# Optimization experiments

Hardware: AMD Instinct MI355X
Metric: run time of the kernel (lower is better)

## Reference

```python
import jax, jax.numpy as jnp
import numpy as np

EPS = 1e-8

def l2norm(x, axis=-1):
    norm = jnp.sqrt(jnp.sum(x * x, axis=axis, keepdims=True)) + EPS
    return x / norm

def setup_inputs() -> dict:
    key = jax.random.key(0)
    ks = jax.random.split(key, 4)
    B, Lq, Ls, d, sim_dim = 128, 128, 256, 1024, 256
    query = jax.random.normal(ks[0], (B, Lq, d), dtype=jnp.float32)
    context = jax.random.normal(ks[1], (B, Ls, d), dtype=jnp.float32)
    matrix = jax.random.uniform(ks[2], (B, Lq, d), dtype=jnp.float32)
    W = jax.random.normal(ks[3], (sim_dim, d), dtype=jnp.float32) * (1.0 / np.sqrt(d))
    b = jnp.zeros((sim_dim,), dtype=jnp.float32)
    smooth = 9
    return {"query": query, "context": context, "matrix": matrix, "W": W, "b": b, "smooth": smooth}

def reference(query, context, matrix, W, b, smooth):
    # cross_attention
    q = query * matrix                                   # (B, Lq, d)
    attn = jnp.einsum('bsd,bqd->bsq', context, q)        # (B, Ls, Lq)
    attn = jnp.where(attn >= 0, attn, 0.1 * attn)        # LeakyReLU(0.1)
    attn = l2norm(attn, axis=-1)                         # normalize over Lq
    attn = jnp.swapaxes(attn, 1, 2)                      # (B, Lq, Ls)
    attn = jax.nn.softmax(attn * smooth, axis=2)         # softmax over source
    wcontext = jnp.einsum('bqs,bsd->bqd', attn, context) # (B, Lq, d)
    wcontext = l2norm(wcontext, axis=-1)
    # alignment vector
    sim_rep = (query - wcontext) ** 2                    # (B, Lq, d)
    sim_rep = jnp.einsum('bqd,kd->bqk', sim_rep, W) + b  # Linear d -> sim_dim
    sim_rep = l2norm(sim_rep, axis=-1)
    return sim_rep
```

## Files before the change

kernel.cpp:

```cpp
#include <hip/hip_runtime.h>
#include <hip/hip_bf16.h>

constexpr int B  = 128;
constexpr int LQ = 128;
constexpr int LS = 256;
constexpr int D  = 1024;
constexpr int SD = 256;
constexpr float EPS = 1e-8f;

typedef __attribute__((ext_vector_type(8))) __bf16 bf16x8;
typedef __attribute__((ext_vector_type(4))) float f32x4;

__device__ inline ushort f2bf(float f) {
    union { float f; uint u; } v{f};
    uint r = v.u + 0x7fffu + ((v.u >> 16) & 1u);
    return (ushort)(r >> 16);
}
__device__ inline float bf2f(ushort u) {
    union { uint u; float f; } v{(uint)u << 16};
    return v.f;
}
__device__ inline uint4 pack8(float4 a, float4 b) {
    union { ushort us[8]; uint4 u4; } r;
    r.us[0]=f2bf(a.x); r.us[1]=f2bf(a.y); r.us[2]=f2bf(a.z); r.us[3]=f2bf(a.w);
    r.us[4]=f2bf(b.x); r.us[5]=f2bf(b.y); r.us[6]=f2bf(b.z); r.us[7]=f2bf(b.w);
    return r.u4;
}
__device__ inline int swz(int row, int kbyte) {
    return row * 128 + (kbyte ^ ((row & 7) << 4));
}
__device__ inline bf16x8 lds_frag(const ushort* base, int row, int kk, int lane) {
    int kbyte = kk * 64 + (lane >> 4) * 16;
    return *(const bf16x8*)((const char*)base + swz(row, kbyte));
}
__device__ inline int swz512(int row, int kbyte) {
    return row * 512 + (kbyte ^ ((row & 7) << 4));
}
__device__ inline f32x4 mfma16(bf16x8 a, bf16x8 b, f32x4 c) {
    return __builtin_amdgcn_mfma_f32_16x16x32_bf16(a, b, c, 0, 0, 0);
}

__global__ __launch_bounds__(256) void wconv_kernel(
    const float* __restrict__ W, ushort* __restrict__ Wb)
{
    size_t i = ((size_t)blockIdx.x * 256 + threadIdx.x) * 8;
    float4 a = *(const float4*)(W + i);
    float4 b = *(const float4*)(W + i + 4);
    *(uint4*)(Wb + i) = pack8(a, b);
}

__global__ __launch_bounds__(512, 2) void gemmA_kernel(
    const float* __restrict__ query, const float* __restrict__ mat,
    const float* __restrict__ ctx, const int* __restrict__ smooth_p,
    ushort* __restrict__ E)
{
    const int bid = blockIdx.x;
    const int xcd = bid & 7, idx = bid >> 3;
    const int b  = xcd * 16 + (idx >> 1);
    const int n0 = (idx & 1) * 128;
    __shared__ ushort SH[4][128 * 64];
    __shared__ float colssP[2][128];
    __shared__ float invsm[128];
    ushort* Et = &SH[0][0];

    const int t = threadIdx.x;
    const int wv = t >> 6, l = t & 63;
    const int wq = wv >> 2, wsv = wv & 3;

    const float* Qb = query + (size_t)b * LQ * D;
    const float* Mb = mat   + (size_t)b * LQ * D;
    const float* Cb = ctx   + ((size_t)b * LS + n0) * D;
    const int r0 = t >> 3, k8 = (t & 7) * 8;

    f32x4 acc[4][2] = {};
    float4 q0,q1,q2,q3, m0,m1,m2,m3, c0,c1,c2,c3;

    auto loadT = [&](int k0) {
        const float* qp = Qb + (size_t)r0 * D + k0 + k8;
        const float* mp = Mb + (size_t)r0 * D + k0 + k8;
        q0 = *(const float4*)qp; q1 = *(const float4*)(qp + 4);
        m0 = *(const float4*)mp; m1 = *(const float4*)(mp + 4);
        qp += (size_t)64 * D;  mp += (size_t)64 * D;
        q2 = *(const float4*)qp; q3 = *(const float4*)(qp + 4);
        m2 = *(const float4*)mp; m3 = *(const float4*)(mp + 4);
        const float* cp = Cb + (size_t)r0 * D + k0 + k8;
        c0 = *(const float4*)cp; c1 = *(const float4*)(cp + 4);
        cp += (size_t)64 * D;
        c2 = *(const float4*)cp; c3 = *(const float4*)(cp + 4);
    };
    auto storeT = [&](int buf) {
        float4 p1{q0.x*m0.x, q0.y*m0.y, q0.z*m0.z, q0.w*m0.w};
        float4 p2{q1.x*m1.x, q1.y*m1.y, q1.z*m1.z, q1.w*m1.w};
        *(uint4*)((char*)&SH[buf][0] + swz(r0, k8 * 2)) = pack8(p1, p2);
        float4 p3{q2.x*m2.x, q2.y*m2.y, q2.z*m2.z, q2.w*m2.w};
        float4 p4{q3.x*m3.x, q3.y*m3.y, q3.z*m3.z, q3.w*m3.w};
        *(uint4*)((char*)&SH[buf][0] + swz(r0 + 64, k8 * 2)) = pack8(p3, p4);
        *(uint4*)((char*)&SH[2 + buf][0] + swz(r0, k8 * 2))      = pack8(c0, c1);
        *(uint4*)((char*)&SH[2 + buf][0] + swz(r0 + 64, k8 * 2)) = pack8(c2, c3);
    };
    auto mfmaT = [&](int buf) {
#pragma unroll
        for (int kk = 0; kk < 2; ++kk) {
            bf16x8 bfr0 = lds_frag(&SH[2 + buf][0], wsv * 32 + (l & 15), kk, l);
            bf16x8 bfr1 = lds_frag(&SH[2 + buf][0], wsv * 32 + 16 + (l & 15), kk, l);
#pragma unroll
            for (int i = 0; i < 4; ++i) {
                bf16x8 af = lds_frag(&SH[buf][0], wq * 64 + i * 16 + (l & 15), kk, l);
                acc[i][0] = mfma16(af, bfr0, acc[i][0]);
                acc[i][1] = mfma16(af, bfr1, acc[i][1]);
            }
        }
    };

    loadT(0);
    storeT(0);
    __syncthreads();
    int cur = 0;
#pragma unroll 1
    for (int ks = 0; ks < 15; ++ks) {
        loadT((ks + 1) * 64);
        mfmaT(cur);
        storeT(cur ^ 1);
        __syncthreads();
        cur ^= 1;
    }
    mfmaT(cur);

#pragma unroll
    for (int n = 0; n < 2; ++n) {
        float csum = 0.f;
#pragma unroll
        for (int i = 0; i < 4; ++i)
#pragma unroll
            for (int r = 0; r < 4; ++r) {
                float v = acc[i][n][r];
                v = v >= 0.f ? v : 0.1f * v;
                acc[i][n][r] = v;
                csum += v * v;
            }
        csum += __shfl_xor(csum, 16);
        csum += __shfl_xor(csum, 32);
        if (l < 16) colssP[wq][wsv * 32 + n * 16 + l] = csum;
    }
    __syncthreads();
    const float sm = (float)(*smooth_p);
    if (t < 128) invsm[t] = sm / (sqrtf(colssP[0][t] + colssP[1][t]) + EPS);
    __syncthreads();
#pragma unroll
    for (int n = 0; n < 2; ++n) {
        const float invc = invsm[wsv * 32 + n * 16 + (l & 15)];
#pragma unroll
        for (int i = 0; i < 4; ++i)
#pragma unroll
            for (int r = 0; r < 4; ++r) {
                int row = wq * 64 + i * 16 + (l >> 4) * 4 + r;
                Et[row * 136 + wsv * 32 + n * 16 + (l & 15)] =
                    f2bf(__expf(acc[i][n][r] * invc));
            }
    }
    __syncthreads();
    ushort* Eg = E + (size_t)b * LQ * LS + n0;
#pragma unroll
    for (int j = 0; j < 4; ++j) {
        int c = t + j * 512;
        int row = c >> 4, s8 = (c & 15) * 8;
        *(uint4*)(Eg + (size_t)row * LS + s8) = *(const uint4*)(Et + row * 136 + s8);
    }
}

__global__ __launch_bounds__(512, 2) void pv_kernel(
    const ushort* __restrict__ E, const float* __restrict__ ctx,
    ushort* __restrict__ wctx, float* __restrict__ rowssP)
{
    const int bid = blockIdx.x;
    const int xcd = bid & 7, idx = bid >> 3;
    const int b  = xcd * 16 + (idx >> 1);
    const int dh = idx & 1;
    const int dglob0 = dh * 512;

    __shared__ ushort Es[128 * 256];
    __shared__ ushort Bs[64 * 264];
    __shared__ float rsumL[128];
    __shared__ float rinv[128];
    __shared__ float rowssL[128][4];

    const int t = threadIdx.x;
    const int wv = t >> 6, l = t & 63;
    const int wq = wv >> 2, wd = wv & 3;

    const ushort* Eb = E + (size_t)b * LQ * LS;
    const int cc = t & 31, rr = t >> 5;
    float part[8];
#pragma unroll
    for (int p = 0; p < 8; ++p) {
        int row = rr + p * 16;
        uint4 v = *(const uint4*)(Eb + (size_t)row * LS + cc * 8);
        *(uint4*)((char*)Es + swz512(row, cc * 16)) = v;
        const ushort* us = (const ushort*)&v;
        float s = 0.f;
#pragma unroll
        for (int j = 0; j < 8; ++j) s += bf2f(us[j]);
        part[p] = s;
    }
    rowssL[t >> 2][t & 3] = 0.f;
#pragma unroll
    for (int p = 0; p < 8; ++p) {
        float s = part[p];
        s += __shfl_xor(s, 1);  s += __shfl_xor(s, 2);
        s += __shfl_xor(s, 4);  s += __shfl_xor(s, 8);
        s += __shfl_xor(s, 16);
        if ((l & 31) == 0) rsumL[rr + p * 16] = s;
    }

    const float* Cb = ctx + (size_t)b * LS * D + dglob0;
    const int sr = t >> 4, c4 = (t & 15) * 4;
    float4 cr[8];
#pragma unroll
    for (int p = 0; p < 8; ++p)
        cr[p] = *(const float4*)(Cb + (size_t)(p * 32 + sr) * D + c4);

    __syncthreads();
    if (t < 128) rinv[t] = 1.0f / rsumL[t];

#pragma unroll
    for (int p = 0; p < 8; ++p) {
        int s = p * 32 + sr;
        Bs[(c4 + 0) * 264 + s] = f2bf(cr[p].x);
        Bs[(c4 + 1) * 264 + s] = f2bf(cr[p].y);
        Bs[(c4 + 2) * 264 + s] = f2bf(cr[p].z);
        Bs[(c4 + 3) * 264 + s] = f2bf(cr[p].w);
    }
    __syncthreads();

    ushort* Ob = wctx + (size_t)b * LQ * D + dglob0;

#pragma unroll 1
    for (int dt = 0; dt < 8; ++dt) {
        if (dt < 7) {
#pragma unroll
            for (int p = 0; p < 8; ++p)
                cr[p] = *(const float4*)(Cb + (size_t)(p * 32 + sr) * D + (dt + 1) * 64 + c4);
        }
        f32x4 acc[4] = {};
#pragma unroll
        for (int kk = 0; kk < 8; ++kk) {
            const ushort* bp = Bs + (wd * 16 + (l & 15)) * 264 + kk * 32 + (l >> 4) * 8;
            bf16x8 bfr = *(const bf16x8*)bp;
#pragma unroll
            for (int i = 0; i < 4; ++i) {
                bf16x8 af = *(const bf16x8*)((const char*)Es +
                    swz512(wq * 64 + i * 16 + (l & 15), kk * 64 + (l >> 4) * 16));
                acc[i] = mfma16(af, bfr, acc[i]);
            }
        }
#pragma unroll
        for (int i = 0; i < 4; ++i)
#pragma unroll
            for (int r = 0; r < 4; ++r) {
                int row = wq * 64 + i * 16 + (l >> 4) * 4 + r;
                float wval = acc[i][r] * rinv[row];
                float p2 = wval * wval;
                p2 += __shfl_xor(p2, 1); p2 += __shfl_xor(p2, 2);
                p2 += __shfl_xor(p2, 4); p2 += __shfl_xor(p2, 8);
                if ((l & 15) == 0) rowssL[row][wd] += p2;
                Ob[(size_t)row * D + dt * 64 + wd * 16 + (l & 15)] = f2bf(wval);
            }
        __syncthreads();
        if (dt < 7) {
#pragma unroll
            for (int p = 0; p < 8; ++p) {
                int s = p * 32 + sr;
                Bs[(c4 + 0) * 264 + s] = f2bf(cr[p].x);
                Bs[(c4 + 1) * 264 + s] = f2bf(cr[p].y);
                Bs[(c4 + 2) * 264 + s] = f2bf(cr[p].z);
                Bs[(c4 + 3) * 264 + s] = f2bf(cr[p].w);
            }
            __syncthreads();
        }
    }
    if (t < 128)
        rowssP[(size_t)b * 256 + dh * 128 + t] =
            rowssL[t][0] + rowssL[t][1] + rowssL[t][2] + rowssL[t][3];
}

__global__ __launch_bounds__(512, 2) void gemm3_kernel(
    const ushort* __restrict__ wctx, const float* __restrict__ query,
    const float* __restrict__ rowssP, const ushort* __restrict__ Wb,
    const float* __restrict__ bias, float* __restrict__ out)
{
    const int m0 = blockIdx.x * 64;
    const int b  = blockIdx.y;
    __shared__ ushort As[64 * 64];
    __shared__ ushort Bs[256 * 64];
    __shared__ float red[64][4];
    __shared__ float invr[64];
    const int t = threadIdx.x;
    const int w = t >> 6, l = t & 63;
    const int wm = (w >> 2) * 32, wn = (w & 3) * 64;

    const int arow = t >> 3, ako = (t & 7) * 8;
    const float r0v = rowssP[(size_t)b * 256 + m0 + arow];
    const float r1v = rowssP[(size_t)b * 256 + 128 + m0 + arow];
    const float ivq = 1.0f / (sqrtf(r0v + r1v) + EPS);
    const float* Qp  = query + ((size_t)b * LQ + m0 + arow) * D + ako;
    const ushort* Wp = wctx  + ((size_t)b * LQ + m0 + arow) * D + ako;

    f32x4 acc[2][4] = {};

    for (int k0 = 0; k0 < D; k0 += 64) {
        if (k0) __syncthreads();
        {
            uint4 wu = *(const uint4*)(Wp + k0);
            float4 q1 = *(const float4*)(Qp + k0);
            float4 q2 = *(const float4*)(Qp + k0 + 4);
            float d0 = q1.x - bf2f((ushort)(wu.x & 0xffff)) * ivq;
            float d1 = q1.y - bf2f((ushort)(wu.x >> 16))    * ivq;
            float d2 = q1.z - bf2f((ushort)(wu.y & 0xffff)) * ivq;
            float d3 = q1.w - bf2f((ushort)(wu.y >> 16))    * ivq;
            float d4 = q2.x - bf2f((ushort)(wu.z & 0xffff)) * ivq;
            float d5 = q2.y - bf2f((ushort)(wu.z >> 16))    * ivq;
            float d6 = q2.z - bf2f((ushort)(wu.w & 0xffff)) * ivq;
            float d7 = q2.w - bf2f((ushort)(wu.w >> 16))    * ivq;
            float4 s1{d0*d0, d1*d1, d2*d2, d3*d3};
            float4 s2{d4*d4, d5*d5, d6*d6, d7*d7};
            *(uint4*)((char*)As + swz(arow, ako * 2)) = pack8(s1, s2);
        }
#pragma unroll
        for (int j = 0; j < 4; ++j) {
            int c = t + j * 512;
            int row = c >> 3, ko = (c & 7) * 8;
            *(uint4*)((char*)Bs + swz(row, ko * 2)) =
                *(const uint4*)(Wb + (size_t)row * D + k0 + ko);
        }
        __syncthreads();
#pragma unroll
        for (int kk = 0; kk < 2; ++kk) {
            bf16x8 af[2], bfr[4];
#pragma unroll
            for (int i = 0; i < 2; ++i) af[i] = lds_frag(As, wm + i * 16 + (l & 15), kk, l);
#pragma unroll
            for (int n = 0; n < 4; ++n) bfr[n] = lds_frag(Bs, wn + n * 16 + (l & 15), kk, l);
#pragma unroll
            for (int i = 0; i < 2; ++i)
#pragma unroll
                for (int n = 0; n < 4; ++n) acc[i][n] = mfma16(af[i], bfr[n], acc[i][n]);
        }
    }
#pragma unroll
    for (int n = 0; n < 4; ++n) {
        float bv = bias[wn + n * 16 + (l & 15)];
#pragma unroll
        for (int i = 0; i < 2; ++i)
#pragma unroll
            for (int r = 0; r < 4; ++r) acc[i][n][r] += bv;
    }
#pragma unroll
    for (int i = 0; i < 2; ++i)
#pragma unroll
        for (int r = 0; r < 4; ++r) {
            float p = 0.f;
#pragma unroll
            for (int n = 0; n < 4; ++n) p += acc[i][n][r] * acc[i][n][r];
#pragma unroll
            for (int off = 1; off < 16; off <<= 1) p += __shfl_xor(p, off);
            int rowl = wm + i * 16 + (l >> 4) * 4 + r;
            if ((l & 15) == 0) red[rowl][w & 3] = p;
        }
    __syncthreads();
    if (t < 64) {
        float s = red[t][0] + red[t][1] + red[t][2] + red[t][3];
        invr[t] = 1.0f / (sqrtf(s) + EPS);
    }
    __syncthreads();
    float* Ob = out + ((size_t)b * LQ + m0) * SD;
#pragma unroll
    for (int i = 0; i < 2; ++i)
#pragma unroll
        for (int r = 0; r < 4; ++r) {
            int rowl = wm + i * 16 + (l >> 4) * 4 + r;
            float iv = invr[rowl];
#pragma unroll
            for (int n = 0; n < 4; ++n) {
                int col = wn + n * 16 + (l & 15);
                Ob[(size_t)rowl * SD + col] = acc[i][n][r] * iv;
            }
        }
}

extern "C" void kernel_launch(void* const* d_in, const int* in_sizes, int n_in,
                              void* d_out, int out_size, void* d_ws, size_t ws_size,
                              hipStream_t stream)
{
    const float* query  = (const float*)d_in[0];
    const float* ctx    = (const float*)d_in[1];
    const float* mat    = (const float*)d_in[2];
    const float* W      = (const float*)d_in[3];
    const float* bias   = (const float*)d_in[4];
    const int*   smooth = (const int*)d_in[5];
    float* out = (float*)d_out;

    char* ws = (char*)d_ws;
    ushort* wctx   = (ushort*)ws;
    ushort* E      = (ushort*)(ws + (size_t)32 * 1024 * 1024);
    ushort* Wb     = (ushort*)(ws + (size_t)40 * 1024 * 1024);
    float*  rowssP = (float*)(ws + (size_t)(40 * 1024 + 512) * 1024);

    wconv_kernel<<<dim3(SD * D / (256 * 8)), 256, 0, stream>>>(W, Wb);
    gemmA_kernel<<<dim3(256), 512, 0, stream>>>(query, mat, ctx, smooth, E);
    pv_kernel<<<dim3(256), 512, 0, stream>>>(E, ctx, wctx, rowssP);
    gemm3_kernel<<<dim3(2, B), 512, 0, stream>>>(wctx, query, rowssP, Wb, bias, out);
}
```

Before: 149.8 us.

## Split gemmA over K into 512 blocks, add combine kernel, reuse bf16 context

```diff
diff --git a/kernel.cpp b/kernel.cpp
--- a/kernel.cpp
+++ b/kernel.cpp
@@ -51,26 +51,28 @@
 
 __global__ __launch_bounds__(512, 2) void gemmA_kernel(
     const float* __restrict__ query, const float* __restrict__ mat,
-    const float* __restrict__ ctx, const int* __restrict__ smooth_p,
-    ushort* __restrict__ E)
+    const float* __restrict__ ctx, float* __restrict__ Spart,
+    ushort* __restrict__ ctxB)
 {
     const int bid = blockIdx.x;
     const int xcd = bid & 7, idx = bid >> 3;
-    const int b  = xcd * 16 + (idx >> 1);
-    const int n0 = (idx & 1) * 128;
+    const int b   = xcd * 16 + (idx >> 2);
+    const int sub = idx & 3;
+    const int sh  = sub >> 1;
+    const int kh  = sub & 1;
+    const int n0    = sh * 128;
+    const int kbase = kh * 512;
     __shared__ ushort SH[4][128 * 64];
-    __shared__ float colssP[2][128];
-    __shared__ float invsm[128];
-    ushort* Et = &SH[0][0];
 
     const int t = threadIdx.x;
+
+    const float* Qb = query + (size_t)b * LQ * D + kbase;
+    const float* Mb = mat   + (size_t)b * LQ * D + kbase;
+    const float* Cb = ctx   + ((size_t)b * LS + n0) * D + kbase;
+    ushort*     CBb = ctxB  + ((size_t)b * LS + n0) * D + kbase;
+    const int r0 = t >> 3, k8 = (t & 7) * 8;
     const int wv = t >> 6, l = t & 63;
     const int wq = wv >> 2, wsv = wv & 3;
-
-    const float* Qb = query + (size_t)b * LQ * D;
-    const float* Mb = mat   + (size_t)b * LQ * D;
-    const float* Cb = ctx   + ((size_t)b * LS + n0) * D;
-    const int r0 = t >> 3, k8 = (t & 7) * 8;
 
     f32x4 acc[4][2] = {};
     float4 q0,q1,q2,q3, m0,m1,m2,m3, c0,c1,c2,c3;
@@ -88,15 +90,19 @@
         cp += (size_t)64 * D;
         c2 = *(const float4*)cp; c3 = *(const float4*)(cp + 4);
     };
-    auto storeT = [&](int buf) {
+    auto storeT = [&](int buf, int kc) {
         float4 p1{q0.x*m0.x, q0.y*m0.y, q0.z*m0.z, q0.w*m0.w};
         float4 p2{q1.x*m1.x, q1.y*m1.y, q1.z*m1.z, q1.w*m1.w};
         *(uint4*)((char*)&SH[buf][0] + swz(r0, k8 * 2)) = pack8(p1, p2);
         float4 p3{q2.x*m2.x, q2.y*m2.y, q2.z*m2.z, q2.w*m2.w};
         float4 p4{q3.x*m3.x, q3.y*m3.y, q3.z*m3.z, q3.w*m3.w};
         *(uint4*)((char*)&SH[buf][0] + swz(r0 + 64, k8 * 2)) = pack8(p3, p4);
-        *(uint4*)((char*)&SH[2 + buf][0] + swz(r0, k8 * 2))      = pack8(c0, c1);
-        *(uint4*)((char*)&SH[2 + buf][0] + swz(r0 + 64, k8 * 2)) = pack8(c2, c3);
+        uint4 pc0 = pack8(c0, c1);
+        uint4 pc1 = pack8(c2, c3);
+        *(uint4*)((char*)&SH[2 + buf][0] + swz(r0, k8 * 2))      = pc0;
+        *(uint4*)((char*)&SH[2 + buf][0] + swz(r0 + 64, k8 * 2)) = pc1;
+        *(uint4*)(CBb + (size_t)r0 * D + kc + k8)        = pc0;
+        *(uint4*)(CBb + (size_t)(r0 + 64) * D + kc + k8) = pc1;
     };
     auto mfmaT = [&](int buf) {
 #pragma unroll
@@ -113,18 +119,53 @@
     };
 
     loadT(0);
-    storeT(0);
+    storeT(0, 0);
     __syncthreads();
     int cur = 0;
 #pragma unroll 1
-    for (int ks = 0; ks < 15; ++ks) {
+    for (int ks = 0; ks < 7; ++ks) {
         loadT((ks + 1) * 64);
         mfmaT(cur);
-        storeT(cur ^ 1);
+        storeT(cur ^ 1, (ks + 1) * 64);
         __syncthreads();
         cur ^= 1;
     }
     mfmaT(cur);
+
+    float* Sp = Spart + (((size_t)(b * 2 + sh) * 2 + kh) * 512 + t) * 32;
+#pragma unroll
+    for (int i = 0; i < 4; ++i)
+#pragma unroll
+        for (int n = 0; n < 2; ++n)
+            *(f32x4*)(Sp + (i * 2 + n) * 4) = acc[i][n];
+}
+
+__global__ __launch_bounds__(512, 2) void combine_kernel(
+    const float* __restrict__ Spart, const int* __restrict__ smooth_p,
+    ushort* __restrict__ E)
+{
+    const int bid = blockIdx.x;
+    const int xcd = bid & 7, idx = bid >> 3;
+    const int b  = xcd * 16 + (idx >> 1);
+    const int sh = idx & 1;
+    __shared__ float colssP[2][128];
+    __shared__ float invsm[128];
+    __shared__ ushort Et[128 * 136];
+
+    const int t = threadIdx.x;
+    const int wv = t >> 6, l = t & 63;
+    const int wq = wv >> 2, wsv = wv & 3;
+
+    const float* S0 = Spart + (((size_t)(b * 2 + sh) * 2 + 0) * 512 + t) * 32;
+    const float* S1 = Spart + (((size_t)(b * 2 + sh) * 2 + 1) * 512 + t) * 32;
+
+    f32x4 acc[4][2];
+#pragma unroll
+    for (int i = 0; i < 4; ++i)
+#pragma unroll
+        for (int n = 0; n < 2; ++n)
+            acc[i][n] = *(const f32x4*)(S0 + (i * 2 + n) * 4) +
+                        *(const f32x4*)(S1 + (i * 2 + n) * 4);
 
 #pragma unroll
     for (int n = 0; n < 2; ++n) {
@@ -159,7 +200,7 @@
             }
     }
     __syncthreads();
-    ushort* Eg = E + (size_t)b * LQ * LS + n0;
+    ushort* Eg = E + (size_t)b * LQ * LS + sh * 128;
 #pragma unroll
     for (int j = 0; j < 4; ++j) {
         int c = t + j * 512;
@@ -169,7 +210,7 @@
 }
 
 __global__ __launch_bounds__(512, 2) void pv_kernel(
-    const ushort* __restrict__ E, const float* __restrict__ ctx,
+    const ushort* __restrict__ E, const ushort* __restrict__ ctxB,
     ushort* __restrict__ wctx, float* __restrict__ rowssP)
 {
     const int bid = blockIdx.x;
@@ -212,12 +253,12 @@
         if ((l & 31) == 0) rsumL[rr + p * 16] = s;
     }
 
-    const float* Cb = ctx + (size_t)b * LS * D + dglob0;
+    const ushort* Cb = ctxB + (size_t)b * LS * D + dglob0;
     const int sr = t >> 4, c4 = (t & 15) * 4;
-    float4 cr[8];
+    uint2 cr[8];
 #pragma unroll
     for (int p = 0; p < 8; ++p)
-        cr[p] = *(const float4*)(Cb + (size_t)(p * 32 + sr) * D + c4);
+        cr[p] = *(const uint2*)(Cb + (size_t)(p * 32 + sr) * D + c4);
 
     __syncthreads();
     if (t < 128) rinv[t] = 1.0f / rsumL[t];
@@ -225,10 +266,11 @@
 #pragma unroll
     for (int p = 0; p < 8; ++p) {
         int s = p * 32 + sr;
-        Bs[(c4 + 0) * 264 + s] = f2bf(cr[p].x);
-        Bs[(c4 + 1) * 264 + s] = f2bf(cr[p].y);
-        Bs[(c4 + 2) * 264 + s] = f2bf(cr[p].z);
-        Bs[(c4 + 3) * 264 + s] = f2bf(cr[p].w);
+        const ushort* us = (const ushort*)&cr[p];
+        Bs[(c4 + 0) * 264 + s] = us[0];
+        Bs[(c4 + 1) * 264 + s] = us[1];
+        Bs[(c4 + 2) * 264 + s] = us[2];
+        Bs[(c4 + 3) * 264 + s] = us[3];
     }
     __syncthreads();
 
@@ -239,7 +281,7 @@
         if (dt < 7) {
 #pragma unroll
             for (int p = 0; p < 8; ++p)
-                cr[p] = *(const float4*)(Cb + (size_t)(p * 32 + sr) * D + (dt + 1) * 64 + c4);
+                cr[p] = *(const uint2*)(Cb + (size_t)(p * 32 + sr) * D + (dt + 1) * 64 + c4);
         }
         f32x4 acc[4] = {};
 #pragma unroll
@@ -270,10 +312,11 @@
 #pragma unroll
             for (int p = 0; p < 8; ++p) {
                 int s = p * 32 + sr;
-                Bs[(c4 + 0) * 264 + s] = f2bf(cr[p].x);
-                Bs[(c4 + 1) * 264 + s] = f2bf(cr[p].y);
-                Bs[(c4 + 2) * 264 + s] = f2bf(cr[p].z);
-                Bs[(c4 + 3) * 264 + s] = f2bf(cr[p].w);
+                const ushort* us = (const ushort*)&cr[p];
+                Bs[(c4 + 0) * 264 + s] = us[0];
+                Bs[(c4 + 1) * 264 + s] = us[1];
+                Bs[(c4 + 2) * 264 + s] = us[2];
+                Bs[(c4 + 3) * 264 + s] = us[3];
             }
             __syncthreads();
         }
@@ -400,13 +443,16 @@
     float* out = (float*)d_out;
 
     char* ws = (char*)d_ws;
-    ushort* wctx   = (ushort*)ws;
-    ushort* E      = (ushort*)(ws + (size_t)32 * 1024 * 1024);
-    ushort* Wb     = (ushort*)(ws + (size_t)40 * 1024 * 1024);
-    float*  rowssP = (float*)(ws + (size_t)(40 * 1024 + 512) * 1024);
+    ushort* ctxB   = (ushort*)ws;
+    float*  Spart  = (float*)(ws + (size_t)64 * 1024 * 1024);
+    ushort* wctx   = (ushort*)Spart;
+    ushort* E      = (ushort*)(ws + (size_t)96 * 1024 * 1024);
+    ushort* Wb     = (ushort*)(ws + (size_t)104 * 1024 * 1024);
+    float*  rowssP = (float*)(ws + (size_t)(104 * 1024 + 512) * 1024);
 
     wconv_kernel<<<dim3(SD * D / (256 * 8)), 256, 0, stream>>>(W, Wb);
-    gemmA_kernel<<<dim3(256), 512, 0, stream>>>(query, mat, ctx, smooth, E);
-    pv_kernel<<<dim3(256), 512, 0, stream>>>(E, ctx, wctx, rowssP);
+    gemmA_kernel<<<dim3(512), 512, 0, stream>>>(query, mat, ctx, Spart, ctxB);
+    combine_kernel<<<dim3(256), 512, 0, stream>>>(Spart, smooth, E);
+    pv_kernel<<<dim3(256), 512, 0, stream>>>(E, ctxB, wctx, rowssP);
     gemm3_kernel<<<dim3(2, B), 512, 0, stream>>>(wctx, query, rowssP, Wb, bias, out);
 }
```

After: 178.8 us. 1.19x slower.

## Stage fp32 tiles to LDS via async global_load_lds and convert at fragment load

Applied to the files above, without the earlier changes.

```diff
diff --git a/kernel.cpp b/kernel.cpp
--- a/kernel.cpp
+++ b/kernel.cpp
@@ -26,6 +26,12 @@
     r.us[4]=f2bf(b.x); r.us[5]=f2bf(b.y); r.us[6]=f2bf(b.z); r.us[7]=f2bf(b.w);
     return r.u4;
 }
+__device__ inline bf16x8 pack8v(float4 a, float4 b) {
+    union { ushort us[8]; bf16x8 v; } r;
+    r.us[0]=f2bf(a.x); r.us[1]=f2bf(a.y); r.us[2]=f2bf(a.z); r.us[3]=f2bf(a.w);
+    r.us[4]=f2bf(b.x); r.us[5]=f2bf(b.y); r.us[6]=f2bf(b.z); r.us[7]=f2bf(b.w);
+    return r.v;
+}
 __device__ inline int swz(int row, int kbyte) {
     return row * 128 + (kbyte ^ ((row & 7) << 4));
 }
@@ -38,6 +44,11 @@
 }
 __device__ inline f32x4 mfma16(bf16x8 a, bf16x8 b, f32x4 c) {
     return __builtin_amdgcn_mfma_f32_16x16x32_bf16(a, b, c, 0, 0, 0);
+}
+__device__ inline void gll16(const void* g, void* l) {
+    __builtin_amdgcn_global_load_lds(
+        (const __attribute__((address_space(1))) void*)g,
+        (__attribute__((address_space(3))) void*)l, 16, 0, 0);
 }
 
 __global__ __launch_bounds__(256) void wconv_kernel(
@@ -57,11 +68,13 @@
     const int bid = blockIdx.x;
     const int xcd = bid & 7, idx = bid >> 3;
     const int b  = xcd * 16 + (idx >> 1);
-    const int n0 = (idx & 1) * 128;
-    __shared__ ushort SH[4][128 * 64];
-    __shared__ float colssP[2][128];
-    __shared__ float invsm[128];
-    ushort* Et = &SH[0][0];
+    const int sh = idx & 1;
+    const int n0 = sh * 128;
+
+    __shared__ __align__(16) char SMEM[96 * 1024 + 1536];
+    float*  colssP = (float*)(SMEM + 98304);
+    float*  invsm  = (float*)(SMEM + 99328);
+    ushort* Et     = (ushort*)SMEM;
 
     const int t = threadIdx.x;
     const int wv = t >> 6, l = t & 63;
@@ -70,61 +83,63 @@
     const float* Qb = query + (size_t)b * LQ * D;
     const float* Mb = mat   + (size_t)b * LQ * D;
     const float* Cb = ctx   + ((size_t)b * LS + n0) * D;
-    const int r0 = t >> 3, k8 = (t & 7) * 8;
+
+    const int r0 = t >> 3,        cr0 = t & 7;
+    const int r1 = (t >> 3) + 64, cr1 = t & 7;
+    const int sc0 = (cr0 ^ (r0 & 7)) * 4;
+    const int sc1 = (cr1 ^ (r1 & 7)) * 4;
+
+    auto stage = [&](int buf, int k0) {
+        char* base = SMEM + buf * 49152;
+        gll16(Qb + (size_t)r0 * D + k0 + sc0, base + t * 16);
+        gll16(Qb + (size_t)r1 * D + k0 + sc1, base + (t + 512) * 16);
+        gll16(Mb + (size_t)r0 * D + k0 + sc0, base + 16384 + t * 16);
+        gll16(Mb + (size_t)r1 * D + k0 + sc1, base + 16384 + (t + 512) * 16);
+        gll16(Cb + (size_t)r0 * D + k0 + sc0, base + 32768 + t * 16);
+        gll16(Cb + (size_t)r1 * D + k0 + sc1, base + 32768 + (t + 512) * 16);
+    };
 
     f32x4 acc[4][2] = {};
-    float4 q0,q1,q2,q3, m0,m1,m2,m3, c0,c1,c2,c3;
-
-    auto loadT = [&](int k0) {
-        const float* qp = Qb + (size_t)r0 * D + k0 + k8;
-        const float* mp = Mb + (size_t)r0 * D + k0 + k8;
-        q0 = *(const float4*)qp; q1 = *(const float4*)(qp + 4);
-        m0 = *(const float4*)mp; m1 = *(const float4*)(mp + 4);
-        qp += (size_t)64 * D;  mp += (size_t)64 * D;
-        q2 = *(const float4*)qp; q3 = *(const float4*)(qp + 4);
-        m2 = *(const float4*)mp; m3 = *(const float4*)(mp + 4);
-        const float* cp = Cb + (size_t)r0 * D + k0 + k8;
-        c0 = *(const float4*)cp; c1 = *(const float4*)(cp + 4);
-        cp += (size_t)64 * D;
-        c2 = *(const float4*)cp; c3 = *(const float4*)(cp + 4);
+    const int kc = (l >> 4) * 2;
+
+    auto compute = [&](int buf) {
+        const char* SQ = SMEM + buf * 49152;
+        const char* SM = SQ + 16384;
+        const char* SC = SQ + 32768;
+        bf16x8 bfr[2];
+#pragma unroll
+        for (int n = 0; n < 2; ++n) {
+            int S = wsv * 32 + n * 16 + (l & 15);
+            float4 cA = *(const float4*)(SC + S * 128 + ((kc ^ (S & 7)) * 16));
+            float4 cB = *(const float4*)(SC + S * 128 + (((kc + 1) ^ (S & 7)) * 16));
+            bfr[n] = pack8v(cA, cB);
+        }
+#pragma unroll
+        for (int i = 0; i < 4; ++i) {
+            int R = wq * 64 + i * 16 + (l & 15);
+            float4 qA = *(const float4*)(SQ + R * 128 + ((kc ^ (R & 7)) * 16));
+            float4 qB = *(const float4*)(SQ + R * 128 + (((kc + 1) ^ (R & 7)) * 16));
+            float4 mA = *(const float4*)(SM + R * 128 + ((kc ^ (R & 7)) * 16));
+            float4 mB = *(const float4*)(SM + R * 128 + (((kc + 1) ^ (R & 7)) * 16));
+            float4 pA{qA.x*mA.x, qA.y*mA.y, qA.z*mA.z, qA.w*mA.w};
+            float4 pB{qB.x*mB.x, qB.y*mB.y, qB.z*mB.z, qB.w*mB.w};
+            bf16x8 af = pack8v(pA, pB);
+            acc[i][0] = mfma16(af, bfr[0], acc[i][0]);
+            acc[i][1] = mfma16(af, bfr[1], acc[i][1]);
+        }
     };
-    auto storeT = [&](int buf) {
-        float4 p1{q0.x*m0.x, q0.y*m0.y, q0.z*m0.z, q0.w*m0.w};
-        float4 p2{q1.x*m1.x, q1.y*m1.y, q1.z*m1.z, q1.w*m1.w};
-        *(uint4*)((char*)&SH[buf][0] + swz(r0, k8 * 2)) = pack8(p1, p2);
-        float4 p3{q2.x*m2.x, q2.y*m2.y, q2.z*m2.z, q2.w*m2.w};
-        float4 p4{q3.x*m3.x, q3.y*m3.y, q3.z*m3.z, q3.w*m3.w};
-        *(uint4*)((char*)&SH[buf][0] + swz(r0 + 64, k8 * 2)) = pack8(p3, p4);
-        *(uint4*)((char*)&SH[2 + buf][0] + swz(r0, k8 * 2))      = pack8(c0, c1);
-        *(uint4*)((char*)&SH[2 + buf][0] + swz(r0 + 64, k8 * 2)) = pack8(c2, c3);
-    };
-    auto mfmaT = [&](int buf) {
-#pragma unroll
-        for (int kk = 0; kk < 2; ++kk) {
-            bf16x8 bfr0 = lds_frag(&SH[2 + buf][0], wsv * 32 + (l & 15), kk, l);
-            bf16x8 bfr1 = lds_frag(&SH[2 + buf][0], wsv * 32 + 16 + (l & 15), kk, l);
-#pragma unroll
-            for (int i = 0; i < 4; ++i) {
-                bf16x8 af = lds_frag(&SH[buf][0], wq * 64 + i * 16 + (l & 15), kk, l);
-                acc[i][0] = mfma16(af, bfr0, acc[i][0]);
-                acc[i][1] = mfma16(af, bfr1, acc[i][1]);
-            }
-        }
-    };
-
-    loadT(0);
-    storeT(0);
+
+    stage(0, 0);
     __syncthreads();
     int cur = 0;
 #pragma unroll 1
-    for (int ks = 0; ks < 15; ++ks) {
-        loadT((ks + 1) * 64);
-        mfmaT(cur);
-        storeT(cur ^ 1);
+    for (int ks = 0; ks < 31; ++ks) {
+        stage(cur ^ 1, (ks + 1) * 32);
+        compute(cur);
         __syncthreads();
         cur ^= 1;
     }
-    mfmaT(cur);
+    compute(cur);
 
 #pragma unroll
     for (int n = 0; n < 2; ++n) {
@@ -140,11 +155,11 @@
             }
         csum += __shfl_xor(csum, 16);
         csum += __shfl_xor(csum, 32);
-        if (l < 16) colssP[wq][wsv * 32 + n * 16 + l] = csum;
+        if (l < 16) colssP[wq * 128 + wsv * 32 + n * 16 + l] = csum;
     }
     __syncthreads();
     const float sm = (float)(*smooth_p);
-    if (t < 128) invsm[t] = sm / (sqrtf(colssP[0][t] + colssP[1][t]) + EPS);
+    if (t < 128) invsm[t] = sm / (sqrtf(colssP[t] + colssP[128 + t]) + EPS);
     __syncthreads();
 #pragma unroll
     for (int n = 0; n < 2; ++n) {
```

New measurement: 160.7 us. +7.3%, slower.
